# Performance work log

Measured on AMD Instinct MI355X. Metric: run time of the kernel, lower is better.

## Reference

```python
import jax, jax.numpy as jnp
import numpy as np

GROUP_SIZE = 128   # GPTQ quantization group size
LORA_SCALING = 32.0 / 16.0  # lora_alpha / r


def setup_inputs() -> dict:
    key = jax.random.key(0)
    k1, k2, k3, k4, k5, k6 = jax.random.split(key, 6)
    B, S, D_in, D_out, R = 4, 2048, 4096, 4096, 16
    n_groups = D_in // GROUP_SIZE
    x = jax.random.normal(k1, (B, S, D_in), dtype=jnp.float32)
    qweight = jax.random.randint(k2, (D_in, D_out), 0, 16, dtype=jnp.int32)
    qzeros = jax.random.randint(k3, (n_groups, D_out), 0, 16, dtype=jnp.int32)
    scales = jax.random.uniform(k4, (n_groups, D_out), dtype=jnp.float32) * 0.01
    lora_A = jax.random.normal(k5, (R, D_in), dtype=jnp.float32) * 0.02
    lora_B = jax.random.normal(k6, (D_out, R), dtype=jnp.float32) * 0.02
    return {"x": x, "qweight": qweight, "qzeros": qzeros,
            "scales": scales, "lora_A": lora_A, "lora_B": lora_B}


def reference(x, qweight, qzeros, scales, lora_A, lora_B):
    # --- GPTQ dequantize: W[i,o] = (q[i,o] - zero[g(i),o]) * scale[g(i),o] ---
    scale_full = jnp.repeat(scales, GROUP_SIZE, axis=0)              # [D_in, D_out]
    zero_full = jnp.repeat(qzeros, GROUP_SIZE, axis=0)               # [D_in, D_out]
    W = (qweight - zero_full).astype(x.dtype) * scale_full           # [D_in, D_out]
    # --- base quantized linear ---
    result = jnp.einsum('bsi,io->bso', x, W)                         # [B, S, D_out]
    # --- LoRA branch (dropout p=0 -> identity): B(A(x)) * scaling ---
    ax = jnp.einsum('bsi,ri->bsr', x, lora_A)                        # [B, S, R]
    lora_out = jnp.einsum('bsr,or->bso', ax, lora_B) * LORA_SCALING  # [B, S, D_out]
    return (result + lora_out).astype(result.dtype)
```

## Files before the change

### kernel.cpp

```cpp
#include <hip/hip_runtime.h>
#include <hip/hip_bf16.h>
#include <stdint.h>

#define D_IN    4096
#define D_OUT   4096
#define M_TOT   8192
#define R_LORA  16
#define SCALING 2.0f

typedef __bf16 bf16x8 __attribute__((ext_vector_type(8)));
typedef float  f32x4  __attribute__((ext_vector_type(4)));
typedef short  s16x8  __attribute__((ext_vector_type(8)));

__device__ __forceinline__ void async_ld16(const void* g, void* l) {
    __builtin_amdgcn_global_load_lds(
        (const __attribute__((address_space(1))) void*)g,
        (__attribute__((address_space(3))) void*)l,
        16, 0, 0);
}

#define BAR() do { asm volatile("" ::: "memory"); \
                   __builtin_amdgcn_s_barrier(); \
                   asm volatile("" ::: "memory"); } while (0)
#define WAIT_VM(n) asm volatile("s_waitcnt vmcnt(" #n ")" ::: "memory")

#define NB_BUILD 4096
#define NB_CVT   16384

__global__ __launch_bounds__(256) void prep(
    const int*   __restrict__ qweight,
    const int*   __restrict__ qzeros,
    const float* __restrict__ scales,
    const float* __restrict__ loraA,
    const float* __restrict__ loraB,
    const float* __restrict__ x,
    __hip_bfloat16* __restrict__ wt,
    __hip_bfloat16* __restrict__ xb)
{
    __shared__ float tile[64][65];
    __shared__ float Abuf[16][64];

    const int b = blockIdx.x;
    const int t = threadIdx.x;

    if (b >= NB_BUILD) {
        size_t idx = ((size_t)(b - NB_BUILD) * 256 + t) * 8;
        f32x4 a = *(const f32x4*)(x + idx);
        f32x4 c = *(const f32x4*)(x + idx + 4);
        union { __hip_bfloat16 h[8]; s16x8 v; } u;
        u.h[0] = __float2bfloat16(a[0]); u.h[1] = __float2bfloat16(a[1]);
        u.h[2] = __float2bfloat16(a[2]); u.h[3] = __float2bfloat16(a[3]);
        u.h[4] = __float2bfloat16(c[0]); u.h[5] = __float2bfloat16(c[1]);
        u.h[6] = __float2bfloat16(c[2]); u.h[7] = __float2bfloat16(c[3]);
        *(s16x8*)(xb + idx) = u.v;
        return;
    }

    const int i0 = (b & 63) * 64;
    const int o0 = (b >> 6) * 64;

    for (int j = t; j < 16 * 64; j += 256) {
        int r = j >> 6, io = j & 63;
        Abuf[r][io] = loraA[r * D_IN + i0 + io];
    }
    const int oo = t & 63;
    const float* bp = loraB + (size_t)(o0 + oo) * R_LORA;
    f32x4 bA = *(const f32x4*)(bp + 0);
    f32x4 bB = *(const f32x4*)(bp + 4);
    f32x4 bC = *(const f32x4*)(bp + 8);
    f32x4 bD = *(const f32x4*)(bp + 12);
    __syncthreads();

    const int g  = i0 >> 7;
    const int   zero = qzeros[g * D_OUT + o0 + oo];
    const float sc   = scales[g * D_OUT + o0 + oo];

    #pragma unroll
    for (int ii = (t >> 6); ii < 64; ii += 4) {
        int q = qweight[(size_t)(i0 + ii) * D_OUT + o0 + oo];
        float w = (float)(q - zero) * sc;
        float acc = 0.f;
        #pragma unroll
        for (int r = 0; r < 4; ++r)
            acc += Abuf[r][ii]      * bA[r] + Abuf[r + 4][ii]  * bB[r]
                 + Abuf[r + 8][ii]  * bC[r] + Abuf[r + 12][ii] * bD[r];
        tile[ii][oo] = w + SCALING * acc;
    }
    __syncthreads();

    const int i_off  = (t & 31) * 2;
    const int o_base = t >> 5;
    #pragma unroll
    for (int p = 0; p < 8; ++p) {
        int o = o_base + p * 8;
        __hip_bfloat162 v;
        v.x = __float2bfloat16(tile[i_off][o]);
        v.y = __float2bfloat16(tile[i_off + 1][o]);
        *(__hip_bfloat162*)&wt[(size_t)(o0 + o) * D_IN + i0 + i_off] = v;
    }
}

#define RDA(fm, ks) (*(const bf16x8*)(aRd + ((fm) * 2 + (ks)) * 1024))
#define RDB(fn, ks) (*(const bf16x8*)(bRd + ((fn) * 2 + (ks)) * 1024))

template<bool LAST>
__device__ __forceinline__ void gemm_tile(
    const char* __restrict__ aRd, const char* __restrict__ bRd,
    char* __restrict__ ldsAn, char* __restrict__ ldsBn,
    const __hip_bfloat16* __restrict__ agA,
    const __hip_bfloat16* __restrict__ agB,
    const int w, const int ub, f32x4 (&acc)[8][4])
{
    bf16x8 af[4][2], bf0[2][2], bf1[2][2];

    #pragma unroll
    for (int fm = 0; fm < 4; ++fm) { af[fm][0] = RDA(fm, 0); af[fm][1] = RDA(fm, 1); }
    #pragma unroll
    for (int fn = 0; fn < 2; ++fn) { bf0[fn][0] = RDB(fn, 0); bf0[fn][1] = RDB(fn, 1); }
    if constexpr (!LAST) {
        async_ld16(agA,                      ldsAn + w * 1024);
        async_ld16(agA + (size_t)128 * D_IN, ldsAn + (16 + w) * 1024);
    }
    if constexpr (LAST) { WAIT_VM(2); } else { WAIT_VM(4); }
    BAR();
    __builtin_amdgcn_s_setprio(1);
    #pragma unroll
    for (int fm = 0; fm < 4; ++fm)
        #pragma unroll
        for (int fn = 0; fn < 2; ++fn)
            #pragma unroll
            for (int ks = 0; ks < 2; ++ks)
                acc[fm][fn] = __builtin_amdgcn_mfma_f32_16x16x32_bf16(
                    af[fm][ks], bf0[fn][ks], acc[fm][fn], 0, 0, 0);
    __builtin_amdgcn_s_setprio(0);

    #pragma unroll
    for (int fn = 0; fn < 2; ++fn) { bf1[fn][0] = RDB(fn + 2, 0); bf1[fn][1] = RDB(fn + 2, 1); }
    if constexpr (!LAST) {
        async_ld16(agB,                      ldsBn + ub * 1024);
        async_ld16(agB + (size_t)128 * D_IN, ldsBn + (ub + 16) * 1024);
    }
    if constexpr (LAST) { WAIT_VM(0); } else { WAIT_VM(4); }
    BAR();
    __builtin_amdgcn_s_setprio(1);
    #pragma unroll
    for (int fm = 0; fm < 4; ++fm)
        #pragma unroll
        for (int fn = 0; fn < 2; ++fn)
            #pragma unroll
            for (int ks = 0; ks < 2; ++ks)
                acc[fm][fn + 2] = __builtin_amdgcn_mfma_f32_16x16x32_bf16(
                    af[fm][ks], bf1[fn][ks], acc[fm][fn + 2], 0, 0, 0);
    __builtin_amdgcn_s_setprio(0);

    #pragma unroll
    for (int fm = 0; fm < 4; ++fm) { af[fm][0] = RDA(fm + 4, 0); af[fm][1] = RDA(fm + 4, 1); }
    if constexpr (!LAST) {
        async_ld16(agB + (size_t)32 * D_IN,  ldsBn + (ub + 4) * 1024);
        async_ld16(agB + (size_t)160 * D_IN, ldsBn + (ub + 20) * 1024);
        async_ld16(agA + (size_t)64 * D_IN,  ldsAn + (8 + w) * 1024);
        async_ld16(agA + (size_t)192 * D_IN, ldsAn + (24 + w) * 1024);
        WAIT_VM(4);
    }
    BAR();
    __builtin_amdgcn_s_setprio(1);
    #pragma unroll
    for (int fm = 0; fm < 4; ++fm)
        #pragma unroll
        for (int fn = 0; fn < 2; ++fn)
            #pragma unroll
            for (int ks = 0; ks < 2; ++ks)
                acc[fm + 4][fn + 2] = __builtin_amdgcn_mfma_f32_16x16x32_bf16(
                    af[fm][ks], bf1[fn][ks], acc[fm + 4][fn + 2], 0, 0, 0);
    #pragma unroll
    for (int fm = 0; fm < 4; ++fm)
        #pragma unroll
        for (int fn = 0; fn < 2; ++fn)
            #pragma unroll
            for (int ks = 0; ks < 2; ++ks)
                acc[fm + 4][fn] = __builtin_amdgcn_mfma_f32_16x16x32_bf16(
                    af[fm][ks], bf0[fn][ks], acc[fm + 4][fn], 0, 0, 0);
    __builtin_amdgcn_s_setprio(0);
}

#define BK 64
#define NKT (D_IN / BK)
#define NWG ((M_TOT / 256) * (D_OUT / 256))

__global__ __launch_bounds__(512) void gemm_xw(
    const __hip_bfloat16* __restrict__ A,
    const __hip_bfloat16* __restrict__ Bt,
    float* __restrict__ C)
{
    extern __shared__ __attribute__((aligned(16))) char lds[];
    char* ldsA = lds;
    char* ldsB = lds + 65536;

    const int t    = threadIdx.x;
    const int lane = t & 63;
    const int w    = t >> 6;
    const int wgm  = w >> 2;
    const int wgn  = w & 3;

    int wg = (int)blockIdx.x;
    wg = (wg & 7) * (NWG / 8) + (wg >> 3);
    const size_t m0 = (size_t)(wg >> 4) * 256;
    const size_t n0 = (size_t)(wg & 15) * 256;

    const int r  = lane & 15;
    const int qq = lane >> 4;

    const size_t arow = m0 + (size_t)(((w >> 1) & 3) * 16 + r);
    const size_t brow = n0 + (size_t)((((w >> 2) & 1) * 4 + ((w >> 1) & 1)) * 16 + r);
    const int    col  = (w & 1) * 32 + qq * 8;
    const __hip_bfloat16* agA = A  + arow * D_IN + col;
    const __hip_bfloat16* agB = Bt + brow * D_IN + col;
    const int ub = (w & 3) + (w >> 2) * 8;

    const char* aRdBase = ldsA + wgm * 16384 + lane * 16;
    const char* bRdBase = ldsB + (wgn >> 1) * 16384 + (wgn & 1) * 8192 + lane * 16;

    f32x4 acc[8][4] = {};

    async_ld16(agA,                      ldsA + w * 1024);
    async_ld16(agA + (size_t)128 * D_IN, ldsA + (16 + w) * 1024);
    async_ld16(agB,                      ldsB + ub * 1024);
    async_ld16(agB + (size_t)128 * D_IN, ldsB + (ub + 16) * 1024);
    async_ld16(agB + (size_t)32 * D_IN,  ldsB + (ub + 4) * 1024);
    async_ld16(agB + (size_t)160 * D_IN, ldsB + (ub + 20) * 1024);
    async_ld16(agA + (size_t)64 * D_IN,  ldsA + (8 + w) * 1024);
    async_ld16(agA + (size_t)192 * D_IN, ldsA + (24 + w) * 1024);
    WAIT_VM(4);
    BAR();

    int p = 0;
    for (int kt = 0; kt < NKT - 1; ++kt) {
        const int kn = (kt + 1) * BK;
        gemm_tile<false>(aRdBase + p * 32768, bRdBase + p * 32768,
                         ldsA + (p ^ 1) * 32768, ldsB + (p ^ 1) * 32768,
                         agA + kn, agB + kn, w, ub, acc);
        p ^= 1;
    }
    gemm_tile<true>(aRdBase + p * 32768, bRdBase + p * 32768,
                    ldsA, ldsB, agA, agB, w, ub, acc);

    const size_t crow0 = m0 + wgm * 128 + qq * 4;
    const size_t ccol0 = n0 + wgn * 64 + r;
    #pragma unroll
    for (int fm = 0; fm < 8; ++fm)
        #pragma unroll
        for (int fn = 0; fn < 4; ++fn)
            #pragma unroll
            for (int e = 0; e < 4; ++e)
                C[(crow0 + fm * 16 + e) * D_OUT + ccol0 + fn * 16] = acc[fm][fn][e];
}

extern "C" void kernel_launch(void* const* d_in, const int* in_sizes, int n_in,
                              void* d_out, int out_size, void* d_ws, size_t ws_size,
                              hipStream_t stream) {
    const float* x       = (const float*)d_in[0];
    const int*   qweight = (const int*)  d_in[1];
    const int*   qzeros  = (const int*)  d_in[2];
    const float* scales  = (const float*)d_in[3];
    const float* loraA   = (const float*)d_in[4];
    const float* loraB   = (const float*)d_in[5];
    float* out = (float*)d_out;

    __hip_bfloat16* wt = (__hip_bfloat16*)d_ws;
    __hip_bfloat16* xb = (__hip_bfloat16*)((char*)d_ws + (size_t)D_OUT * D_IN * 2);

    static bool attr_set = false;
    if (!attr_set) {
        hipFuncSetAttribute(reinterpret_cast<const void*>(gemm_xw),
                            hipFuncAttributeMaxDynamicSharedMemorySize, 131072);
        attr_set = true;
    }

    prep<<<dim3(NB_BUILD + NB_CVT), 256, 0, stream>>>(
        qweight, qzeros, scales, loraA, loraB, x, wt, xb);
    gemm_xw<<<dim3(NWG), 512, 131072, stream>>>(xb, wt, out);
}
```

Measured before the change: 522.8 us.

## Software-pipeline LDS fragment loads across MFMA clusters and stage epilogue through LDS

Restructures the GEMM tile loop so LDS fragment reads for the next MFMA cluster, including the next k-tile's A fragments, are issued between clusters and carried in registers across iterations. Barrier and vmcnt waits are moved so loads overlap with MFMAs. The epilogue writes accumulators through a per-wave LDS slab so global stores become 16-byte row-contiguous vectors, and launch bounds request 2 waves per SIMD. The extra live fragment registers may add pressure against the occupancy hint and could cause spills.

```diff
diff --git a/kernel.cpp b/kernel.cpp
--- a/kernel.cpp
+++ b/kernel.cpp
@@ -100,61 +100,62 @@
     }
 }
 
-#define RDA(fm, ks) (*(const bf16x8*)(aRd + ((fm) * 2 + (ks)) * 1024))
-#define RDB(fn, ks) (*(const bf16x8*)(bRd + ((fn) * 2 + (ks)) * 1024))
+#define MFMA_CL(ACC, AF, BF)                                              \
+    _Pragma("unroll")                                                     \
+    for (int fm = 0; fm < 4; ++fm)                                        \
+        _Pragma("unroll")                                                 \
+        for (int fn = 0; fn < 2; ++fn)                                    \
+            _Pragma("unroll")                                             \
+            for (int ks = 0; ks < 2; ++ks)                                \
+                ACC = __builtin_amdgcn_mfma_f32_16x16x32_bf16(            \
+                    AF[fm][ks], BF[fn][ks], ACC, 0, 0, 0);
 
 template<bool LAST>
 __device__ __forceinline__ void gemm_tile(
     const char* __restrict__ aRd, const char* __restrict__ bRd,
+    const char* __restrict__ aRdN,
     char* __restrict__ ldsAn, char* __restrict__ ldsBn,
     const __hip_bfloat16* __restrict__ agA,
     const __hip_bfloat16* __restrict__ agB,
-    const int w, const int ub, f32x4 (&acc)[8][4])
+    const int w, const int ub,
+    bf16x8 (&afA)[4][2], bf16x8 (&afB)[4][2],
+    bf16x8 (&bf0)[2][2], bf16x8 (&bf1)[2][2], f32x4 (&acc)[8][4])
 {
-    bf16x8 af[4][2], bf0[2][2], bf1[2][2];
-
-    #pragma unroll
-    for (int fm = 0; fm < 4; ++fm) { af[fm][0] = RDA(fm, 0); af[fm][1] = RDA(fm, 1); }
-    #pragma unroll
-    for (int fn = 0; fn < 2; ++fn) { bf0[fn][0] = RDB(fn, 0); bf0[fn][1] = RDB(fn, 1); }
     if constexpr (!LAST) {
         async_ld16(agA,                      ldsAn + w * 1024);
         async_ld16(agA + (size_t)128 * D_IN, ldsAn + (16 + w) * 1024);
-    }
-    if constexpr (LAST) { WAIT_VM(2); } else { WAIT_VM(4); }
-    BAR();
-    __builtin_amdgcn_s_setprio(1);
-    #pragma unroll
-    for (int fm = 0; fm < 4; ++fm)
-        #pragma unroll
-        for (int fn = 0; fn < 2; ++fn)
-            #pragma unroll
-            for (int ks = 0; ks < 2; ++ks)
-                acc[fm][fn] = __builtin_amdgcn_mfma_f32_16x16x32_bf16(
-                    af[fm][ks], bf0[fn][ks], acc[fm][fn], 0, 0, 0);
-    __builtin_amdgcn_s_setprio(0);
-
-    #pragma unroll
-    for (int fn = 0; fn < 2; ++fn) { bf1[fn][0] = RDB(fn + 2, 0); bf1[fn][1] = RDB(fn + 2, 1); }
+        WAIT_VM(4);
+    } else { WAIT_VM(2); }
+    BAR();
+    #pragma unroll
+    for (int fn = 0; fn < 2; ++fn) {
+        bf0[fn][0] = *(const bf16x8*)(bRd + (fn * 2 + 0) * 1024);
+        bf0[fn][1] = *(const bf16x8*)(bRd + (fn * 2 + 1) * 1024);
+    }
+    #pragma unroll
+    for (int fn = 0; fn < 2; ++fn) {
+        bf1[fn][0] = *(const bf16x8*)(bRd + ((fn + 2) * 2 + 0) * 1024);
+        bf1[fn][1] = *(const bf16x8*)(bRd + ((fn + 2) * 2 + 1) * 1024);
+    }
+    __builtin_amdgcn_s_setprio(1);
+    MFMA_CL(acc[fm][fn], afA, bf0);
+    __builtin_amdgcn_s_setprio(0);
+
     if constexpr (!LAST) {
         async_ld16(agB,                      ldsBn + ub * 1024);
         async_ld16(agB + (size_t)128 * D_IN, ldsBn + (ub + 16) * 1024);
-    }
-    if constexpr (LAST) { WAIT_VM(0); } else { WAIT_VM(4); }
-    BAR();
-    __builtin_amdgcn_s_setprio(1);
-    #pragma unroll
-    for (int fm = 0; fm < 4; ++fm)
-        #pragma unroll
-        for (int fn = 0; fn < 2; ++fn)
-            #pragma unroll
-            for (int ks = 0; ks < 2; ++ks)
-                acc[fm][fn + 2] = __builtin_amdgcn_mfma_f32_16x16x32_bf16(
-                    af[fm][ks], bf1[fn][ks], acc[fm][fn + 2], 0, 0, 0);
-    __builtin_amdgcn_s_setprio(0);
-
-    #pragma unroll
-    for (int fm = 0; fm < 4; ++fm) { af[fm][0] = RDA(fm + 4, 0); af[fm][1] = RDA(fm + 4, 1); }
+        WAIT_VM(4);
+    } else { WAIT_VM(0); }
+    BAR();
+    __builtin_amdgcn_s_setprio(1);
+    MFMA_CL(acc[fm][fn + 2], afA, bf1);
+    __builtin_amdgcn_s_setprio(0);
+    #pragma unroll
+    for (int fm = 0; fm < 4; ++fm) {
+        afB[fm][0] = *(const bf16x8*)(aRd + ((fm + 4) * 2 + 0) * 1024);
+        afB[fm][1] = *(const bf16x8*)(aRd + ((fm + 4) * 2 + 1) * 1024);
+    }
+
     if constexpr (!LAST) {
         async_ld16(agB + (size_t)32 * D_IN,  ldsBn + (ub + 4) * 1024);
         async_ld16(agB + (size_t)160 * D_IN, ldsBn + (ub + 20) * 1024);
@@ -164,22 +165,17 @@
     }
     BAR();
     __builtin_amdgcn_s_setprio(1);
-    #pragma unroll
-    for (int fm = 0; fm < 4; ++fm)
-        #pragma unroll
-        for (int fn = 0; fn < 2; ++fn)
-            #pragma unroll
-            for (int ks = 0; ks < 2; ++ks)
-                acc[fm + 4][fn + 2] = __builtin_amdgcn_mfma_f32_16x16x32_bf16(
-                    af[fm][ks], bf1[fn][ks], acc[fm + 4][fn + 2], 0, 0, 0);
-    #pragma unroll
-    for (int fm = 0; fm < 4; ++fm)
-        #pragma unroll
-        for (int fn = 0; fn < 2; ++fn)
-            #pragma unroll
-            for (int ks = 0; ks < 2; ++ks)
-                acc[fm + 4][fn] = __builtin_amdgcn_mfma_f32_16x16x32_bf16(
-                    af[fm][ks], bf0[fn][ks], acc[fm + 4][fn], 0, 0, 0);
+    MFMA_CL(acc[fm + 4][fn], afB, bf0);
+    __builtin_amdgcn_s_setprio(0);
+    if constexpr (!LAST) {
+        #pragma unroll
+        for (int fm = 0; fm < 4; ++fm) {
+            afA[fm][0] = *(const bf16x8*)(aRdN + (fm * 2 + 0) * 1024);
+            afA[fm][1] = *(const bf16x8*)(aRdN + (fm * 2 + 1) * 1024);
+        }
+    }
+    __builtin_amdgcn_s_setprio(1);
+    MFMA_CL(acc[fm + 4][fn + 2], afB, bf1);
     __builtin_amdgcn_s_setprio(0);
 }
 
@@ -187,7 +183,7 @@
 #define NKT (D_IN / BK)
 #define NWG ((M_TOT / 256) * (D_OUT / 256))
 
-__global__ __launch_bounds__(512) void gemm_xw(
+__global__ __launch_bounds__(512, 2) void gemm_xw(
     const __hip_bfloat16* __restrict__ A,
     const __hip_bfloat16* __restrict__ Bt,
     float* __restrict__ C)
@@ -221,6 +217,7 @@
     const char* bRdBase = ldsB + (wgn >> 1) * 16384 + (wgn & 1) * 8192 + lane * 16;
 
     f32x4 acc[8][4] = {};
+    bf16x8 afA[4][2], afB[4][2], bf0[2][2], bf1[2][2];
 
     async_ld16(agA,                      ldsA + w * 1024);
     async_ld16(agA + (size_t)128 * D_IN, ldsA + (16 + w) * 1024);
@@ -230,29 +227,46 @@
     async_ld16(agB + (size_t)160 * D_IN, ldsB + (ub + 20) * 1024);
     async_ld16(agA + (size_t)64 * D_IN,  ldsA + (8 + w) * 1024);
     async_ld16(agA + (size_t)192 * D_IN, ldsA + (24 + w) * 1024);
-    WAIT_VM(4);
-    BAR();
+    WAIT_VM(6);
+    BAR();
+    #pragma unroll
+    for (int fm = 0; fm < 4; ++fm) {
+        afA[fm][0] = *(const bf16x8*)(aRdBase + (fm * 2 + 0) * 1024);
+        afA[fm][1] = *(const bf16x8*)(aRdBase + (fm * 2 + 1) * 1024);
+    }
 
     int p = 0;
     for (int kt = 0; kt < NKT - 1; ++kt) {
         const int kn = (kt + 1) * BK;
         gemm_tile<false>(aRdBase + p * 32768, bRdBase + p * 32768,
+                         aRdBase + (p ^ 1) * 32768,
                          ldsA + (p ^ 1) * 32768, ldsB + (p ^ 1) * 32768,
-                         agA + kn, agB + kn, w, ub, acc);
+                         agA + kn, agB + kn, w, ub, afA, afB, bf0, bf1, acc);
         p ^= 1;
     }
     gemm_tile<true>(aRdBase + p * 32768, bRdBase + p * 32768,
-                    ldsA, ldsB, agA, agB, w, ub, acc);
-
-    const size_t crow0 = m0 + wgm * 128 + qq * 4;
-    const size_t ccol0 = n0 + wgn * 64 + r;
-    #pragma unroll
-    for (int fm = 0; fm < 8; ++fm)
+                    aRdBase, ldsA, ldsB, agA, agB, w, ub,
+                    afA, afB, bf0, bf1, acc);
+
+    BAR();
+    float* slab = (float*)(lds + w * 4352);
+    const size_t crow0 = m0 + wgm * 128;
+    const size_t ccol0 = n0 + wgn * 64;
+    const int rr = lane >> 4;
+    const int cc = lane & 15;
+    #pragma unroll
+    for (int fm = 0; fm < 8; ++fm) {
         #pragma unroll
         for (int fn = 0; fn < 4; ++fn)
             #pragma unroll
             for (int e = 0; e < 4; ++e)
-                C[(crow0 + fm * 16 + e) * D_OUT + ccol0 + fn * 16] = acc[fm][fn][e];
+                slab[(qq * 4 + e) * 68 + fn * 16 + r] = acc[fm][fn][e];
+        #pragma unroll
+        for (int j = 0; j < 4; ++j) {
+            f32x4 v = *(const f32x4*)(slab + (j * 4 + rr) * 68 + cc * 4);
+            *(f32x4*)&C[(crow0 + fm * 16 + j * 4 + rr) * D_OUT + ccol0 + cc * 4] = v;
+        }
+    }
 }
 
 extern "C" void kernel_launch(void* const* d_in, const int* in_sizes, int n_in,
```

Measured after the change: 525.9 us. No clear change (+0.6%).
